# Optimization experiments

Hardware: AMD Instinct MI355X
Metric: run time of the kernel (lower is better)

Reference implementation:

```python
import jax, jax.numpy as jnp
import numpy as np

T, B, C = 256, 512, 128
NA = 4  # num attentions


def _lin(key, fan_in, fan_out):
    kw, kb = jax.random.split(key)
    s = 1.0 / np.sqrt(fan_in)
    W = jax.random.uniform(kw, (fan_in, fan_out), jnp.float32, -s, s)
    b = jax.random.uniform(kb, (fan_out,), jnp.float32, -s, s)
    return W, b


def setup_inputs() -> dict:
    key = jax.random.key(0)
    ks = jax.random.split(key, 12)
    inp = {
        'eeg': jax.random.normal(ks[0], (T, B, C), jnp.float32),
        'eog': jax.random.normal(ks[1], (T, B, C), jnp.float32),
    }
    # LSTHM (shared across both modalities)
    inp['Ww'], inp['Wb'] = _lin(ks[2], C, 4 * C)
    inp['Uw'], inp['Ub'] = _lin(ks[3], C, 4 * C)
    inp['Vw'], inp['Vb'] = _lin(ks[4], C, 4 * C)
    # attention model: Linear(256,128) -> tanh -> Linear(128,1024)
    inp['A1'], inp['a1'] = _lin(ks[5], 2 * C, C)
    inp['A2'], inp['a2'] = _lin(ks[6], C, NA * 2 * C)
    # dim-reduce nets: Linear(512,128) -> tanh -> Linear(128,128), one per modality
    inp['D10'], inp['e10'] = _lin(ks[7], NA * C, C)
    inp['D20'], inp['e20'] = _lin(ks[8], C, C)
    inp['D11'], inp['e11'] = _lin(ks[9], NA * C, C)
    inp['D21'], inp['e21'] = _lin(ks[10], C, C)
    return inp


def reference(eeg, eog, Ww, Wb, Uw, Ub, Vw, Vb, A1, a1, A2, a2,
              D10, e10, D20, e20, D11, e11, D21, e21):
    def mlp(x, W1, b1, W2, b2):
        return jnp.tanh(x @ W1 + b1) @ W2 + b2

    def lsthm(x, c, h, z, first):
        # at t=0 the torch code zeroes the U/V affines entirely (biases included)
        sums = (x @ Ww + Wb) + jnp.where(first, 0.0, (h @ Uw + Ub) + (z @ Vw + Vb))
        f = jax.nn.sigmoid(sums[:, :C])
        i = jax.nn.sigmoid(sums[:, C:2 * C])
        o = jax.nn.sigmoid(sums[:, 2 * C:3 * C])
        ch = jnp.tanh(sums[:, 3 * C:])
        c_t = f * c + i * ch
        h_t = jnp.tanh(c_t) * o
        return c_t, h_t

    def step(carry, inp):
        c0, h0, c1, h1, z0, z1 = carry
        x0, x1, first = inp
        c0, h0 = lsthm(x0, c0, h0, z0, first)
        c1, h1 = lsthm(x1, c1, h1, z1, first)
        in_t = jnp.concatenate([h0, h1], axis=1)                       # [B, 2C]
        logits = mlp(in_t, A1, a1, A2, a2)                             # [B, NA*2C]
        atts = jax.nn.softmax(logits.reshape(-1, NA, 2 * C), axis=1)   # softmax over attentions
        atts = atts.reshape(-1, NA * 2 * C)
        out_t = jnp.concatenate([jnp.tile(h0, (1, NA)), jnp.tile(h1, (1, NA))], axis=1)
        att = atts * out_t                                             # [B, NA*2C]
        z0 = mlp(att[:, :NA * C], D10, e10, D20, e20)
        z1 = mlp(att[:, NA * C:], D11, e11, D21, e21)
        out = jnp.concatenate([z0, z1], axis=1)                        # [B, 2C]
        return (c0, h0, c1, h1, z0, z1), out

    zeros = jnp.zeros((eeg.shape[1], C), eeg.dtype)
    first = jnp.arange(eeg.shape[0]) == 0
    _, outs = jax.lax.scan(step, (zeros,) * 6, (eeg, eog, first))
    return outs  # [T, B, 2C]
```

## Files before the change

kernel.cpp:

```cpp
#include <hip/hip_runtime.h>

typedef unsigned short u16;
typedef unsigned int   u32;
typedef __attribute__((ext_vector_type(8))) __bf16 bf16x8;
typedef __attribute__((ext_vector_type(4))) float  f32x4;

#define T_STEPS 256
#define BATCH   512
#define RB      16
#define NBLK    32

__device__ __forceinline__ float b2f(u16 u){
  union { u32 i; float f; } v; v.i = ((u32)u) << 16; return v.f;
}
__device__ __forceinline__ u16 f2b(float f){
  u32 x = __float_as_uint(f);
  return (u16)((x + 0x7fffu + ((x >> 16) & 1u)) >> 16);
}
__device__ __forceinline__ float sigm_f(float x){ return 1.f/(1.f + __expf(-x)); }
__device__ __forceinline__ float tanh_f(float x){
  x = fminf(15.f, fmaxf(-15.f, x));
  float e = __expf(2.f*x);
  return (e - 1.f)/(e + 1.f);
}
__device__ __forceinline__ f32x4 MF(bf16x8 a, bf16x8 b, f32x4 c){
  return __builtin_amdgcn_mfma_f32_16x16x32_bf16(a, b, c, 0, 0, 0);
}

__device__ __forceinline__ bf16x8 frA(const u16* buf, int l, int kc, int RS){
  int r = l & 15;
  int byte = r*RS + kc*64 + ((l >> 4) << 4);
  byte ^= (r & 7) << 4;
  return *(const bf16x8*)((const char*)buf + byte);
}
__device__ __forceinline__ void st16(u16* buf, int r, int c, u16 v, int RS){
  int byte = r*RS + c*2; byte ^= (r & 7) << 4;
  *(u16*)((char*)buf + byte) = v;
}
__device__ __forceinline__ float ld16f(const u16* buf, int r, int c, int RS){
  int byte = r*RS + c*2; byte ^= (r & 7) << 4;
  return b2f(*(const u16*)((const char*)buf + byte));
}
__device__ __forceinline__ void st16x4(u16* buf, int r, int c, ushort4 v, int RS){
  int byte = r*RS + c*2; byte ^= (r & 7) << 4;
  *(ushort4*)((char*)buf + byte) = v;
}
__device__ __forceinline__ bf16x8 frB(const u16* pk, int nt, int kt, int KT, int l){
  return *(const bf16x8*)(pk + ((((nt*KT + kt) << 6) + l) << 3));
}

__global__ void pack_w(const float* __restrict__ src, u16* __restrict__ dst,
                       int Ksrc, int N, int ktOff, int KT)
{
  int i = blockIdx.x*256 + threadIdx.x;
  if (i >= Ksrc*N) return;
  int j = i & 7, l = (i >> 3) & 63, p = i >> 9;
  int nkt = Ksrc >> 5;
  int kt = p % nkt, nt = p / nkt;
  int k = (kt << 5) + ((l >> 4) << 3) + j;
  int n = (nt << 4) + (l & 15);
  dst[(((nt*KT + ktOff + kt) << 6) + l)*8 + j] = f2b(src[(size_t)k*N + n]);
}

__global__ void pack_bias(const float* Wb, const float* Ub, const float* Vb,
                          const float* a1, const float* a2,
                          const float* e10, const float* e20,
                          const float* e11, const float* e21, float* bout)
{
  int i = blockIdx.x*256 + threadIdx.x;
  if (i >= 2688) return;
  float v;
  if      (i < 512)  v = Wb[i];
  else if (i < 1024) { int n = i - 512; v = Wb[n] + Ub[n] + Vb[n]; }
  else if (i < 1152) v = a1[i - 1024];
  else if (i < 2176) v = a2[i - 1152];
  else if (i < 2304) v = e10[i - 2176];
  else if (i < 2432) v = e20[i - 2304];
  else if (i < 2560) v = e11[i - 2432];
  else               v = e21[i - 2560];
  bout[i] = v;
}

__global__ __launch_bounds__(512, 2) void marn_mfma5(
  const float* __restrict__ eeg, const float* __restrict__ eog,
  const u16* __restrict__ UVWt, const u16* __restrict__ A1t,
  const u16* __restrict__ A2t,  const u16* __restrict__ D10t,
  const u16* __restrict__ D20t, const u16* __restrict__ D11t,
  const u16* __restrict__ D21t, const float* __restrict__ bias,
  float* __restrict__ out)
{
  __shared__ u16  aS1[2][16*384];
  __shared__ u16  aS2a[16*256];
  __shared__ u16  aS2b[16*128];
  __shared__ u16  aS3a[2][16*512];
  __shared__ u16  aS3b[2][16*128];
  __shared__ float bsh[2688];

  const int tid = threadIdx.x;
  const int w = tid >> 6, l = tid & 63;
  const int hi = l >> 4, li = l & 15;
  const int r0 = blockIdx.x * RB;

  for (int i = tid; i < 2688; i += 512) bsh[i] = bias[i];
  for (int i = tid; i < 2*16*384; i += 512) ((u16*)aS1)[i] = 0;
  float cst[2][4] = {{0,0,0,0},{0,0,0,0}};

  const int xi = tid << 3;
  const int xm = xi >> 11, xrr = (xi >> 7) & 15, xc = xi & 127;
  const float* xsrc = (xm ? eog : eeg) + ((size_t)(r0 + xrr))*128 + xc;
  f32x4 xa = __builtin_nontemporal_load((const f32x4*)xsrc);
  f32x4 xb = __builtin_nontemporal_load((const f32x4*)(xsrc + 4));
  __syncthreads();
  {
    ushort4 va, vb;
    va.x = f2b(xa[0]); va.y = f2b(xa[1]); va.z = f2b(xa[2]); va.w = f2b(xa[3]);
    vb.x = f2b(xb[0]); vb.y = f2b(xb[1]); vb.z = f2b(xb[2]); vb.w = f2b(xb[3]);
    st16x4(&aS1[xm][0], xrr, xc,     va, 768);
    st16x4(&aS1[xm][0], xrr, xc + 4, vb, 768);
  }
  __syncthreads();

  for (int t = 0; t < T_STEPS; ++t){
    f32x4 ac0[4] = {{0,0,0,0},{0,0,0,0},{0,0,0,0},{0,0,0,0}};
    f32x4 ac1[4] = {{0,0,0,0},{0,0,0,0},{0,0,0,0},{0,0,0,0}};
    {
      #pragma unroll
      for (int kc = 0; kc < 12; ++kc){
        bf16x8 fa0 = frA(&aS1[0][0], l, kc, 768);
        bf16x8 fa1 = frA(&aS1[1][0], l, kc, 768);
        #pragma unroll
        for (int g = 0; g < 4; ++g){
          bf16x8 b = frB(UVWt, w + 8*g, kc, 12, l);
          ac0[g] = MF(fa0, b, ac0[g]);
          ac1[g] = MF(fa1, b, ac1[g]);
        }
      }
    }
    __syncthreads();

    {
      const float* bg = bsh + (t == 0 ? 0 : 512);
      const int col = w*16 + li;
      #pragma unroll
      for (int jr = 0; jr < 4; ++jr){
        const int row = hi*4 + jr;
        {
          float f  = sigm_f(ac0[0][jr] + bg[col]);
          float ii = sigm_f(ac0[1][jr] + bg[128+col]);
          float o  = sigm_f(ac0[2][jr] + bg[256+col]);
          float ch = tanh_f(ac0[3][jr] + bg[384+col]);
          cst[0][jr] = f*cst[0][jr] + ii*ch;
          u16 hb = f2b(tanh_f(cst[0][jr])*o);
          st16(&aS1[0][0], row, 128 + col, hb, 768);
          st16(aS2a, row, col, hb, 512);
        }
        {
          float f  = sigm_f(ac1[0][jr] + bg[col]);
          float ii = sigm_f(ac1[1][jr] + bg[128+col]);
          float o  = sigm_f(ac1[2][jr] + bg[256+col]);
          float ch = tanh_f(ac1[3][jr] + bg[384+col]);
          cst[1][jr] = f*cst[1][jr] + ii*ch;
          u16 hb = f2b(tanh_f(cst[1][jr])*o);
          st16(&aS1[1][0], row, 128 + col, hb, 768);
          st16(aS2a, row, 128 + col, hb, 512);
        }
      }
    }
    __syncthreads();

    {
      f32x4 acc = {0,0,0,0};
      #pragma unroll
      for (int kc = 0; kc < 8; ++kc)
        acc = MF(frA(aS2a, l, kc, 512), frB(A1t, w, kc, 8, l), acc);
      const int col = w*16 + li;
      #pragma unroll
      for (int jr = 0; jr < 4; ++jr)
        st16(aS2b, hi*4 + jr, col, f2b(tanh_f(acc[jr] + bsh[1024 + col])), 256);
    }
    __syncthreads();

    {
      int tn = (t + 1 < T_STEPS) ? t + 1 : t;
      xa = __builtin_nontemporal_load((const f32x4*)(xsrc + (size_t)tn*BATCH*128));
      xb = __builtin_nontemporal_load((const f32x4*)(xsrc + (size_t)tn*BATCH*128 + 4));
    }

    {
      bf16x8 yf[4];
      #pragma unroll
      for (int kc = 0; kc < 4; ++kc) yf[kc] = frA(aS2b, l, kc, 256);
      const float* a2f = bsh + 1152;
      #pragma unroll
      for (int gq = 0; gq < 2; ++gq){
        const int gb = w + 8*gq;
        f32x4 q0 = {0,0,0,0}, q1 = {0,0,0,0}, q2 = {0,0,0,0}, q3 = {0,0,0,0};
        #pragma unroll
        for (int kc = 0; kc < 4; ++kc){
          q0 = MF(yf[kc], frB(A2t, gb,      kc, 4, l), q0);
          q1 = MF(yf[kc], frB(A2t, gb + 16, kc, 4, l), q1);
          q2 = MF(yf[kc], frB(A2t, gb + 32, kc, 4, l), q2);
          q3 = MF(yf[kc], frB(A2t, gb + 48, kc, 4, l), q3);
        }
        const int g = gb*16 + li;
        #pragma unroll
        for (int jr = 0; jr < 4; ++jr){
          const int row = hi*4 + jr;
          float v0 = q0[jr] + a2f[g];
          float v1 = q1[jr] + a2f[256 + g];
          float v2 = q2[jr] + a2f[512 + g];
          float v3 = q3[jr] + a2f[768 + g];
          float mx = fmaxf(fmaxf(v0,v1), fmaxf(v2,v3));
          float e0 = __expf(v0-mx), e1 = __expf(v1-mx);
          float e2 = __expf(v2-mx), e3 = __expf(v3-mx);
          float inv = 1.f/(e0+e1+e2+e3);
          float h0v = ld16f(aS2a, row, g & 127, 512);
          float h1v = ld16f(aS2a, row, 128 + (g & 127), 512);
          st16(&aS3a[0][0], row, g,       f2b(e0*inv*h0v), 1024);
          st16(&aS3a[0][0], row, 256 + g, f2b(e1*inv*h0v), 1024);
          st16(&aS3a[1][0], row, g,       f2b(e2*inv*h1v), 1024);
          st16(&aS3a[1][0], row, 256 + g, f2b(e3*inv*h1v), 1024);
        }
      }
    }
    __syncthreads();

    {
      #pragma unroll
      for (int m = 0; m < 2; ++m){
        const u16* Dt = m ? D11t : D10t;
        f32x4 acc = {0,0,0,0};
        #pragma unroll
        for (int kc = 0; kc < 16; ++kc)
          acc = MF(frA(&aS3a[m][0], l, kc, 1024), frB(Dt, w, kc, 16, l), acc);
        const int col = w*16 + li;
        const float* e1f = bsh + (m ? 2432 : 2176);
        #pragma unroll
        for (int jr = 0; jr < 4; ++jr)
          st16(&aS3b[m][0], hi*4 + jr, col, f2b(tanh_f(acc[jr] + e1f[col])), 256);
      }
    }
    __syncthreads();

    {
      #pragma unroll
      for (int m = 0; m < 2; ++m){
        const u16* Dt = m ? D21t : D20t;
        f32x4 acc = {0,0,0,0};
        #pragma unroll
        for (int kc = 0; kc < 4; ++kc)
          acc = MF(frA(&aS3b[m][0], l, kc, 256), frB(Dt, w, kc, 4, l), acc);
        const int col = w*16 + li;
        const float* e2f = bsh + (m ? 2560 : 2304);
        #pragma unroll
        for (int jr = 0; jr < 4; ++jr){
          const int row = hi*4 + jr;
          float z = acc[jr] + e2f[col];
          __builtin_nontemporal_store(z, &out[((size_t)t*BATCH + r0 + row)*256 + m*128 + col]);
          st16(&aS1[m][0], row, 256 + col, f2b(z), 768);
        }
      }
    }
    {
      ushort4 va, vb;
      va.x = f2b(xa[0]); va.y = f2b(xa[1]); va.z = f2b(xa[2]); va.w = f2b(xa[3]);
      vb.x = f2b(xb[0]); vb.y = f2b(xb[1]); vb.z = f2b(xb[2]); vb.w = f2b(xb[3]);
      st16x4(&aS1[xm][0], xrr, xc,     va, 768);
      st16x4(&aS1[xm][0], xrr, xc + 4, vb, 768);
    }
    __syncthreads();
  }
}

extern "C" void kernel_launch(void* const* d_in, const int* in_sizes, int n_in,
                              void* d_out, int out_size, void* d_ws, size_t ws_size,
                              hipStream_t stream)
{
  const float* eeg = (const float*)d_in[0];
  const float* eog = (const float*)d_in[1];
  const float* Ww  = (const float*)d_in[2];
  const float* Wb  = (const float*)d_in[3];
  const float* Uw  = (const float*)d_in[4];
  const float* Ub  = (const float*)d_in[5];
  const float* Vw  = (const float*)d_in[6];
  const float* Vb  = (const float*)d_in[7];
  const float* A1  = (const float*)d_in[8];
  const float* a1  = (const float*)d_in[9];
  const float* A2  = (const float*)d_in[10];
  const float* a2  = (const float*)d_in[11];
  const float* D10 = (const float*)d_in[12];
  const float* e10 = (const float*)d_in[13];
  const float* D20 = (const float*)d_in[14];
  const float* e20 = (const float*)d_in[15];
  const float* D11 = (const float*)d_in[16];
  const float* e11 = (const float*)d_in[17];
  const float* D21 = (const float*)d_in[18];
  const float* e21 = (const float*)d_in[19];

  char* ws = (char*)d_ws;
  u16*  UVWt = (u16*)(ws);
  u16*  A1t  = (u16*)(ws + 393216);
  u16*  A2t  = (u16*)(ws + 458752);
  u16*  D10t = (u16*)(ws + 720896);
  u16*  D20t = (u16*)(ws + 851968);
  u16*  D11t = (u16*)(ws + 884736);
  u16*  D21t = (u16*)(ws + 1015808);
  float* bias = (float*)(ws + 1048576);

  auto nb = [](int n){ return dim3((unsigned)((n + 255)/256)); };
  pack_w<<<nb(65536),  256, 0, stream>>>(Ww,  UVWt, 128, 512,  0, 12);
  pack_w<<<nb(65536),  256, 0, stream>>>(Uw,  UVWt, 128, 512,  4, 12);
  pack_w<<<nb(65536),  256, 0, stream>>>(Vw,  UVWt, 128, 512,  8, 12);
  pack_w<<<nb(32768),  256, 0, stream>>>(A1,  A1t,  256, 128,  0, 8);
  pack_w<<<nb(131072), 256, 0, stream>>>(A2,  A2t,  128, 1024, 0, 4);
  pack_w<<<nb(65536),  256, 0, stream>>>(D10, D10t, 512, 128,  0, 16);
  pack_w<<<nb(16384),  256, 0, stream>>>(D20, D20t, 128, 128,  0, 4);
  pack_w<<<nb(65536),  256, 0, stream>>>(D11, D11t, 512, 128,  0, 16);
  pack_w<<<nb(16384),  256, 0, stream>>>(D21, D21t, 128, 128,  0, 4);
  pack_bias<<<nb(2688), 256, 0, stream>>>(Wb, Ub, Vb, a1, a2, e10, e20, e11, e21, bias);

  marn_mfma5<<<NBLK, 512, 0, stream>>>(eeg, eog, UVWt, A1t, A2t,
                                       D10t, D20t, D11t, D21t, bias, (float*)d_out);
}
```

Baseline: 7.106 ms.

## Prefetch weight fragments into registers across barriers and use LDS-only barrier waits

Global weight fragments for each GEMM stage (UVW, A1, A2, D1x, D2x) are now loaded into registers one phase ahead, before the preceding barrier, so their latency overlaps the previous stage's compute. The UVW loop is double-buffered in blocks of three k-chunks. __syncthreads is replaced by a barrier that waits only on LDS counters, so outstanding global loads need not drain. The cost is much higher register pressure, which under launch_bounds(512,2) could cause spills.

New measurement: 7.105 ms. About the same (-0.0%).

```diff
diff --git a/kernel.cpp b/kernel.cpp
--- a/kernel.cpp
+++ b/kernel.cpp
@@ -25,6 +25,10 @@
 }
 __device__ __forceinline__ f32x4 MF(bf16x8 a, bf16x8 b, f32x4 c){
   return __builtin_amdgcn_mfma_f32_16x16x32_bf16(a, b, c, 0, 0, 0);
+}
+__device__ __forceinline__ void BAR(){
+  asm volatile("s_waitcnt lgkmcnt(0)" ::: "memory");
+  __builtin_amdgcn_s_barrier();
 }
 
 __device__ __forceinline__ bf16x8 frA(const u16* buf, int l, int kc, int RS){
@@ -81,7 +85,7 @@
   bout[i] = v;
 }
 
-__global__ __launch_bounds__(512, 2) void marn_mfma5(
+__global__ __launch_bounds__(512, 2) void marn_mfma6(
   const float* __restrict__ eeg, const float* __restrict__ eog,
   const u16* __restrict__ UVWt, const u16* __restrict__ A1t,
   const u16* __restrict__ A2t,  const u16* __restrict__ D10t,
@@ -124,19 +128,40 @@
     f32x4 ac0[4] = {{0,0,0,0},{0,0,0,0},{0,0,0,0},{0,0,0,0}};
     f32x4 ac1[4] = {{0,0,0,0},{0,0,0,0},{0,0,0,0},{0,0,0,0}};
     {
-      #pragma unroll
-      for (int kc = 0; kc < 12; ++kc){
-        bf16x8 fa0 = frA(&aS1[0][0], l, kc, 768);
-        bf16x8 fa1 = frA(&aS1[1][0], l, kc, 768);
-        #pragma unroll
-        for (int g = 0; g < 4; ++g){
-          bf16x8 b = frB(UVWt, w + 8*g, kc, 12, l);
-          ac0[g] = MF(fa0, b, ac0[g]);
-          ac1[g] = MF(fa1, b, ac1[g]);
-        }
-      }
-    }
-    __syncthreads();
+      bf16x8 wb0[12], wb1[12];
+      #pragma unroll
+      for (int j = 0; j < 3; ++j)
+        #pragma unroll
+        for (int g = 0; g < 4; ++g)
+          wb0[j*4+g] = frB(UVWt, w + 8*g, j, 12, l);
+      #pragma unroll
+      for (int blk = 0; blk < 4; ++blk){
+        bf16x8* cur = (blk & 1) ? wb1 : wb0;
+        bf16x8* nxt = (blk & 1) ? wb0 : wb1;
+        if (blk < 3){
+          #pragma unroll
+          for (int j = 0; j < 3; ++j)
+            #pragma unroll
+            for (int g = 0; g < 4; ++g)
+              nxt[j*4+g] = frB(UVWt, w + 8*g, 3*blk + 3 + j, 12, l);
+        }
+        #pragma unroll
+        for (int j = 0; j < 3; ++j){
+          const int kc = 3*blk + j;
+          bf16x8 fa0 = frA(&aS1[0][0], l, kc, 768);
+          bf16x8 fa1 = frA(&aS1[1][0], l, kc, 768);
+          #pragma unroll
+          for (int g = 0; g < 4; ++g){
+            ac0[g] = MF(fa0, cur[j*4+g], ac0[g]);
+            ac1[g] = MF(fa1, cur[j*4+g], ac1[g]);
+          }
+        }
+      }
+    }
+    bf16x8 wa1[8];
+    #pragma unroll
+    for (int kc = 0; kc < 8; ++kc) wa1[kc] = frB(A1t, w, kc, 8, l);
+    BAR();
 
     {
       const float* bg = bsh + (t == 0 ? 0 : 512);
@@ -166,50 +191,63 @@
         }
       }
     }
-    __syncthreads();
+    bf16x8 wa2A[16];
+    #pragma unroll
+    for (int s = 0; s < 4; ++s)
+      #pragma unroll
+      for (int kc = 0; kc < 4; ++kc)
+        wa2A[s*4+kc] = frB(A2t, w + 16*s, kc, 4, l);
+    BAR();
 
     {
       f32x4 acc = {0,0,0,0};
       #pragma unroll
       for (int kc = 0; kc < 8; ++kc)
-        acc = MF(frA(aS2a, l, kc, 512), frB(A1t, w, kc, 8, l), acc);
+        acc = MF(frA(aS2a, l, kc, 512), wa1[kc], acc);
       const int col = w*16 + li;
       #pragma unroll
       for (int jr = 0; jr < 4; ++jr)
         st16(aS2b, hi*4 + jr, col, f2b(tanh_f(acc[jr] + bsh[1024 + col])), 256);
     }
-    __syncthreads();
-
+    bf16x8 wa2B[16];
+    #pragma unroll
+    for (int s = 0; s < 4; ++s)
+      #pragma unroll
+      for (int kc = 0; kc < 4; ++kc)
+        wa2B[s*4+kc] = frB(A2t, w + 8 + 16*s, kc, 4, l);
     {
       int tn = (t + 1 < T_STEPS) ? t + 1 : t;
       xa = __builtin_nontemporal_load((const f32x4*)(xsrc + (size_t)tn*BATCH*128));
       xb = __builtin_nontemporal_load((const f32x4*)(xsrc + (size_t)tn*BATCH*128 + 4));
     }
+    BAR();
 
     {
       bf16x8 yf[4];
       #pragma unroll
       for (int kc = 0; kc < 4; ++kc) yf[kc] = frA(aS2b, l, kc, 256);
       const float* a2f = bsh + 1152;
+      f32x4 qq[8];
+      #pragma unroll
+      for (int s = 0; s < 8; ++s) qq[s] = (f32x4){0,0,0,0};
+      #pragma unroll
+      for (int s = 0; s < 4; ++s)
+        #pragma unroll
+        for (int kc = 0; kc < 4; ++kc){
+          qq[s]     = MF(yf[kc], wa2A[s*4+kc], qq[s]);
+          qq[4 + s] = MF(yf[kc], wa2B[s*4+kc], qq[4 + s]);
+        }
       #pragma unroll
       for (int gq = 0; gq < 2; ++gq){
         const int gb = w + 8*gq;
-        f32x4 q0 = {0,0,0,0}, q1 = {0,0,0,0}, q2 = {0,0,0,0}, q3 = {0,0,0,0};
-        #pragma unroll
-        for (int kc = 0; kc < 4; ++kc){
-          q0 = MF(yf[kc], frB(A2t, gb,      kc, 4, l), q0);
-          q1 = MF(yf[kc], frB(A2t, gb + 16, kc, 4, l), q1);
-          q2 = MF(yf[kc], frB(A2t, gb + 32, kc, 4, l), q2);
-          q3 = MF(yf[kc], frB(A2t, gb + 48, kc, 4, l), q3);
-        }
         const int g = gb*16 + li;
         #pragma unroll
         for (int jr = 0; jr < 4; ++jr){
           const int row = hi*4 + jr;
-          float v0 = q0[jr] + a2f[g];
-          float v1 = q1[jr] + a2f[256 + g];
-          float v2 = q2[jr] + a2f[512 + g];
-          float v3 = q3[jr] + a2f[768 + g];
+          float v0 = qq[4*gq + 0][jr] + a2f[g];
+          float v1 = qq[4*gq + 1][jr] + a2f[256 + g];
+          float v2 = qq[4*gq + 2][jr] + a2f[512 + g];
+          float v3 = qq[4*gq + 3][jr] + a2f[768 + g];
           float mx = fmaxf(fmaxf(v0,v1), fmaxf(v2,v3));
           float e0 = __expf(v0-mx), e1 = __expf(v1-mx);
           float e2 = __expf(v2-mx), e3 = __expf(v3-mx);
@@ -223,41 +261,73 @@
         }
       }
     }
-    __syncthreads();
-
-    {
-      #pragma unroll
-      for (int m = 0; m < 2; ++m){
-        const u16* Dt = m ? D11t : D10t;
+    bf16x8 wd0[16];
+    #pragma unroll
+    for (int kc = 0; kc < 16; ++kc) wd0[kc] = frB(D10t, w, kc, 16, l);
+    BAR();
+
+    {
+      bf16x8 wd1[16];
+      #pragma unroll
+      for (int kc = 0; kc < 16; ++kc) wd1[kc] = frB(D11t, w, kc, 16, l);
+      const int col = w*16 + li;
+      {
         f32x4 acc = {0,0,0,0};
         #pragma unroll
         for (int kc = 0; kc < 16; ++kc)
-          acc = MF(frA(&aS3a[m][0], l, kc, 1024), frB(Dt, w, kc, 16, l), acc);
-        const int col = w*16 + li;
-        const float* e1f = bsh + (m ? 2432 : 2176);
+          acc = MF(frA(&aS3a[0][0], l, kc, 1024), wd0[kc], acc);
+        const float* e1f = bsh + 2176;
         #pragma unroll
         for (int jr = 0; jr < 4; ++jr)
-          st16(&aS3b[m][0], hi*4 + jr, col, f2b(tanh_f(acc[jr] + e1f[col])), 256);
-      }
-    }
-    __syncthreads();
-
-    {
-      #pragma unroll
-      for (int m = 0; m < 2; ++m){
-        const u16* Dt = m ? D21t : D20t;
+          st16(&aS3b[0][0], hi*4 + jr, col, f2b(tanh_f(acc[jr] + e1f[col])), 256);
+      }
+      {
         f32x4 acc = {0,0,0,0};
         #pragma unroll
+        for (int kc = 0; kc < 16; ++kc)
+          acc = MF(frA(&aS3a[1][0], l, kc, 1024), wd1[kc], acc);
+        const float* e1f = bsh + 2432;
+        #pragma unroll
+        for (int jr = 0; jr < 4; ++jr)
+          st16(&aS3b[1][0], hi*4 + jr, col, f2b(tanh_f(acc[jr] + e1f[col])), 256);
+      }
+    }
+    bf16x8 wd2m0[4], wd2m1[4];
+    #pragma unroll
+    for (int kc = 0; kc < 4; ++kc){
+      wd2m0[kc] = frB(D20t, w, kc, 4, l);
+      wd2m1[kc] = frB(D21t, w, kc, 4, l);
+    }
+    BAR();
+
+    {
+      const int col = w*16 + li;
+      {
+        f32x4 acc = {0,0,0,0};
+        #pragma unroll
         for (int kc = 0; kc < 4; ++kc)
-          acc = MF(frA(&aS3b[m][0], l, kc, 256), frB(Dt, w, kc, 4, l), acc);
-        const int col = w*16 + li;
-        const float* e2f = bsh + (m ? 2560 : 2304);
+          acc = MF(frA(&aS3b[0][0], l, kc, 256), wd2m0[kc], acc);
+        const float* e2f = bsh + 2304;
         #pragma unroll
         for (int jr = 0; jr < 4; ++jr){
           const int row = hi*4 + jr;
           float z = acc[jr] + e2f[col];
-          __builtin_nontemporal_store(z, &out[((size_t)t*BATCH + r0 + row)*256 + m*128 + col]);
-          st16(&aS1[m][0], row, 256 + col, f2b(z), 768);
+          __builtin_nontemporal_store(z, &out[((size_t)t*BATCH + r0 + row)*256 + col]);
+          st16(&aS1[0][0], row, 256 + col, f2b(z), 768);
+        }
+      }
+      {
+        f32x4 acc = {0,0,0,0};
+        #pragma unroll
+        for (int kc = 0; kc < 4; ++kc)
+          acc = MF(frA(&aS3b[1][0], l, kc, 256), wd2m1[kc], acc);
+        const float* e2f = bsh + 2560;
+        #pragma unroll
+        for (int jr = 0; jr < 4; ++jr){
+          const int row = hi*4 + jr;
+          float z = acc[jr] + e2f[col];
+          __builtin_nontemporal_store(z, &out[((size_t)t*BATCH + r0 + row)*256 + 128 + col]);
+          st16(&aS1[1][0], row, 256 + col, f2b(z), 768);
         }
       }
     }
@@ -268,7 +338,7 @@
       st16x4(&aS1[xm][0], xrr, xc,     va, 768);
       st16x4(&aS1[xm][0], xrr, xc + 4, vb, 768);
     }
-    __syncthreads();
+    BAR();
   }
 }
 
@@ -319,6 +389,6 @@
   pack_w<<<nb(16384),  256, 0, stream>>>(D21, D21t, 128, 128,  0, 4);
   pack_bias<<<nb(2688), 256, 0, stream>>>(Wb, Ub, Vb, a1, a2, e10, e20, e11, e21, bias);
 
-  marn_mfma5<<<NBLK, 512, 0, stream>>>(eeg, eog, UVWt, A1t, A2t,
+  marn_mfma6<<<NBLK, 512, 0, stream>>>(eeg, eog, UVWt, A1t, A2t,
                                        D10t, D20t, D11t, D21t, bias, (float*)d_out);
 }
```

## Stream weights through per-wave LDS ring via async global-to-LDS DMA

Applied to the files above, without the earlier changes.

Replaces direct global loads of packed weight fragments with a per-wave double-buffered LDS ring filled by global_load_lds DMA. Each k-chunk's weights are prefetched two chunks ahead across every stage, including across timesteps. The code manages this with explicit vmcnt/lgkmcnt waits and raw s_barrier in place of __syncthreads. Biases now live in registers instead of a shared array, and the next-timestep input prefetch is moved into the D1 stage. This aims to hide the L2 latency of the weight reads on the serial recurrence, at the cost of fragile hand-counted waitcnt logic and an extra 64KB of LDS.

After: 6.608 ms. -7.0%, faster.

```diff
diff --git a/kernel.cpp b/kernel.cpp
--- a/kernel.cpp
+++ b/kernel.cpp
@@ -9,6 +9,9 @@
 #define BATCH   512
 #define RB      16
 #define NBLK    32
+
+#define WAITV(N) asm volatile("s_waitcnt vmcnt(" #N ")" ::: "memory")
+#define LGKM0    asm volatile("s_waitcnt lgkmcnt(0)" ::: "memory")
 
 __device__ __forceinline__ float b2f(u16 u){
   union { u32 i; float f; } v; v.i = ((u32)u) << 16; return v.f;
@@ -26,6 +29,31 @@
 __device__ __forceinline__ f32x4 MF(bf16x8 a, bf16x8 b, f32x4 c){
   return __builtin_amdgcn_mfma_f32_16x16x32_bf16(a, b, c, 0, 0, 0);
 }
+__device__ __forceinline__ void BAR(){
+  asm volatile("s_waitcnt lgkmcnt(0)" ::: "memory");
+  __builtin_amdgcn_s_barrier();
+}
+
+__device__ __forceinline__ void dma16(const u16* g, u16* l){
+  __builtin_amdgcn_global_load_lds(
+      (const __attribute__((address_space(1))) void*)g,
+      (__attribute__((address_space(3))) void*)l, 16, 0, 0);
+}
+__device__ __forceinline__ void issueG(const u16* f0, const u16* f1,
+                                       const u16* f2, const u16* f3,
+                                       u16* ringW, int par, int l){
+  u16* s = ringW + par*2048;
+  dma16(f0 + l*8, s);
+  dma16(f1 + l*8, s + 512);
+  dma16(f2 + l*8, s + 1024);
+  dma16(f3 + l*8, s + 1536);
+}
+__device__ __forceinline__ const u16* fp(const u16* pk, int nt, int kt, int KT){
+  return pk + (size_t)(nt*KT + kt)*512;
+}
+__device__ __forceinline__ bf16x8 rdW(const u16* ringW, int par, int j, int l){
+  return *(const bf16x8*)(ringW + par*2048 + j*512 + l*8);
+}
 
 __device__ __forceinline__ bf16x8 frA(const u16* buf, int l, int kc, int RS){
   int r = l & 15;
@@ -44,9 +72,6 @@
 __device__ __forceinline__ void st16x4(u16* buf, int r, int c, ushort4 v, int RS){
   int byte = r*RS + c*2; byte ^= (r & 7) << 4;
   *(ushort4*)((char*)buf + byte) = v;
-}
-__device__ __forceinline__ bf16x8 frB(const u16* pk, int nt, int kt, int KT, int l){
-  return *(const bf16x8*)(pk + ((((nt*KT + kt) << 6) + l) << 3));
 }
 
 __global__ void pack_w(const float* __restrict__ src, u16* __restrict__ dst,
@@ -81,7 +106,7 @@
   bout[i] = v;
 }
 
-__global__ __launch_bounds__(512, 2) void marn_mfma5(
+__global__ __launch_bounds__(512, 2) void marn_dma(
   const float* __restrict__ eeg, const float* __restrict__ eog,
   const u16* __restrict__ UVWt, const u16* __restrict__ A1t,
   const u16* __restrict__ A2t,  const u16* __restrict__ D10t,
@@ -89,21 +114,35 @@
   const u16* __restrict__ D21t, const float* __restrict__ bias,
   float* __restrict__ out)
 {
-  __shared__ u16  aS1[2][16*384];
-  __shared__ u16  aS2a[16*256];
-  __shared__ u16  aS2b[16*128];
-  __shared__ u16  aS3a[2][16*512];
-  __shared__ u16  aS3b[2][16*128];
-  __shared__ float bsh[2688];
+  __shared__ u16 aS1[2][16*384];
+  __shared__ u16 aS2a[16*256];
+  __shared__ u16 aS2b[16*128];
+  __shared__ u16 aS3a[2][16*512];
+  __shared__ u16 aS3b[2][16*128];
+  __shared__ u16 ring[8][4096];
 
   const int tid = threadIdx.x;
   const int w = tid >> 6, l = tid & 63;
   const int hi = l >> 4, li = l & 15;
   const int r0 = blockIdx.x * RB;
-
-  for (int i = tid; i < 2688; i += 512) bsh[i] = bias[i];
+  u16* ringW = &ring[w][0];
+
   for (int i = tid; i < 2*16*384; i += 512) ((u16*)aS1)[i] = 0;
   float cst[2][4] = {{0,0,0,0},{0,0,0,0}};
+
+  const int col = w*16 + li;
+  const int g1c = (w + 8)*16 + li;
+  float bW[4], bA[4], a2b0[4], a2b1[4];
+  #pragma unroll
+  for (int q = 0; q < 4; ++q){
+    bW[q]   = bias[q*128 + col];
+    bA[q]   = bias[512 + q*128 + col];
+    a2b0[q] = bias[1152 + q*256 + col];
+    a2b1[q] = bias[1152 + q*256 + g1c];
+  }
+  const float a1b  = bias[1024 + col];
+  const float e1b0 = bias[2176 + col], e1b1 = bias[2432 + col];
+  const float e2b0 = bias[2304 + col], e2b1 = bias[2560 + col];
 
   const int xi = tid << 3;
   const int xm = xi >> 11, xrr = (xi >> 7) & 15, xc = xi & 127;
@@ -120,45 +159,56 @@
   }
   __syncthreads();
 
+  issueG(fp(UVWt,w,0,12), fp(UVWt,w+8,0,12), fp(UVWt,w+16,0,12), fp(UVWt,w+24,0,12), ringW, 0, l);
+  issueG(fp(UVWt,w,1,12), fp(UVWt,w+8,1,12), fp(UVWt,w+16,1,12), fp(UVWt,w+24,1,12), ringW, 1, l);
+
   for (int t = 0; t < T_STEPS; ++t){
     f32x4 ac0[4] = {{0,0,0,0},{0,0,0,0},{0,0,0,0},{0,0,0,0}};
     f32x4 ac1[4] = {{0,0,0,0},{0,0,0,0},{0,0,0,0},{0,0,0,0}};
-    {
-      #pragma unroll
-      for (int kc = 0; kc < 12; ++kc){
-        bf16x8 fa0 = frA(&aS1[0][0], l, kc, 768);
-        bf16x8 fa1 = frA(&aS1[1][0], l, kc, 768);
-        #pragma unroll
-        for (int g = 0; g < 4; ++g){
-          bf16x8 b = frB(UVWt, w + 8*g, kc, 12, l);
-          ac0[g] = MF(fa0, b, ac0[g]);
-          ac1[g] = MF(fa1, b, ac1[g]);
-        }
-      }
-    }
-    __syncthreads();
-
-    {
-      const float* bg = bsh + (t == 0 ? 0 : 512);
-      const int col = w*16 + li;
+    #pragma unroll
+    for (int kc = 0; kc < 12; ++kc){
+      WAITV(4);
+      bf16x8 b0 = rdW(ringW, kc&1, 0, l);
+      bf16x8 b1 = rdW(ringW, kc&1, 1, l);
+      bf16x8 b2 = rdW(ringW, kc&1, 2, l);
+      bf16x8 b3 = rdW(ringW, kc&1, 3, l);
+      bf16x8 fa0 = frA(&aS1[0][0], l, kc, 768);
+      bf16x8 fa1 = frA(&aS1[1][0], l, kc, 768);
+      ac0[0] = MF(fa0, b0, ac0[0]);  ac1[0] = MF(fa1, b0, ac1[0]);
+      ac0[1] = MF(fa0, b1, ac0[1]);  ac1[1] = MF(fa1, b1, ac1[1]);
+      ac0[2] = MF(fa0, b2, ac0[2]);  ac1[2] = MF(fa1, b2, ac1[2]);
+      ac0[3] = MF(fa0, b3, ac0[3]);  ac1[3] = MF(fa1, b3, ac1[3]);
+      LGKM0;
+      if (kc < 10){
+        const int k2 = kc + 2;
+        issueG(fp(UVWt,w,k2,12), fp(UVWt,w+8,k2,12), fp(UVWt,w+16,k2,12), fp(UVWt,w+24,k2,12), ringW, k2&1, l);
+      } else if (kc == 10){
+        issueG(fp(A1t,w,0,8), fp(A1t,w,1,8), fp(A1t,w,2,8), fp(A1t,w,3,8), ringW, 0, l);
+      } else {
+        issueG(fp(A1t,w,4,8), fp(A1t,w,5,8), fp(A1t,w,6,8), fp(A1t,w,7,8), ringW, 1, l);
+      }
+    }
+    BAR();
+
+    {
       #pragma unroll
       for (int jr = 0; jr < 4; ++jr){
         const int row = hi*4 + jr;
         {
-          float f  = sigm_f(ac0[0][jr] + bg[col]);
-          float ii = sigm_f(ac0[1][jr] + bg[128+col]);
-          float o  = sigm_f(ac0[2][jr] + bg[256+col]);
-          float ch = tanh_f(ac0[3][jr] + bg[384+col]);
+          float f  = sigm_f(ac0[0][jr] + (t==0 ? bW[0] : bA[0]));
+          float ii = sigm_f(ac0[1][jr] + (t==0 ? bW[1] : bA[1]));
+          float o  = sigm_f(ac0[2][jr] + (t==0 ? bW[2] : bA[2]));
+          float ch = tanh_f(ac0[3][jr] + (t==0 ? bW[3] : bA[3]));
           cst[0][jr] = f*cst[0][jr] + ii*ch;
           u16 hb = f2b(tanh_f(cst[0][jr])*o);
           st16(&aS1[0][0], row, 128 + col, hb, 768);
           st16(aS2a, row, col, hb, 512);
         }
         {
-          float f  = sigm_f(ac1[0][jr] + bg[col]);
-          float ii = sigm_f(ac1[1][jr] + bg[128+col]);
-          float o  = sigm_f(ac1[2][jr] + bg[256+col]);
-          float ch = tanh_f(ac1[3][jr] + bg[384+col]);
+          float f  = sigm_f(ac1[0][jr] + (t==0 ? bW[0] : bA[0]));
+          float ii = sigm_f(ac1[1][jr] + (t==0 ? bW[1] : bA[1]));
+          float o  = sigm_f(ac1[2][jr] + (t==0 ? bW[2] : bA[2]));
+          float ch = tanh_f(ac1[3][jr] + (t==0 ? bW[3] : bA[3]));
           cst[1][jr] = f*cst[1][jr] + ii*ch;
           u16 hb = f2b(tanh_f(cst[1][jr])*o);
           st16(&aS1[1][0], row, 128 + col, hb, 768);
@@ -166,50 +216,63 @@
         }
       }
     }
-    __syncthreads();
-
-    {
-      f32x4 acc = {0,0,0,0};
-      #pragma unroll
-      for (int kc = 0; kc < 8; ++kc)
-        acc = MF(frA(aS2a, l, kc, 512), frB(A1t, w, kc, 8, l), acc);
-      const int col = w*16 + li;
+    BAR();
+
+    {
+      f32x4 accA = {0,0,0,0};
+      WAITV(4);
+      #pragma unroll
+      for (int j = 0; j < 4; ++j)
+        accA = MF(frA(aS2a, l, j, 512), rdW(ringW, 0, j, l), accA);
+      LGKM0;
+      issueG(fp(A2t,w,0,4), fp(A2t,w,1,4), fp(A2t,w,2,4), fp(A2t,w,3,4), ringW, 0, l);
+      WAITV(4);
+      #pragma unroll
+      for (int j = 0; j < 4; ++j)
+        accA = MF(frA(aS2a, l, 4+j, 512), rdW(ringW, 1, j, l), accA);
+      LGKM0;
+      issueG(fp(A2t,w+16,0,4), fp(A2t,w+16,1,4), fp(A2t,w+16,2,4), fp(A2t,w+16,3,4), ringW, 1, l);
       #pragma unroll
       for (int jr = 0; jr < 4; ++jr)
-        st16(aS2b, hi*4 + jr, col, f2b(tanh_f(acc[jr] + bsh[1024 + col])), 256);
-    }
-    __syncthreads();
-
-    {
-      int tn = (t + 1 < T_STEPS) ? t + 1 : t;
-      xa = __builtin_nontemporal_load((const f32x4*)(xsrc + (size_t)tn*BATCH*128));
-      xb = __builtin_nontemporal_load((const f32x4*)(xsrc + (size_t)tn*BATCH*128 + 4));
-    }
+        st16(aS2b, hi*4 + jr, col, f2b(tanh_f(accA[jr] + a1b)), 256);
+    }
+    BAR();
 
     {
       bf16x8 yf[4];
       #pragma unroll
       for (int kc = 0; kc < 4; ++kc) yf[kc] = frA(aS2b, l, kc, 256);
-      const float* a2f = bsh + 1152;
+      f32x4 qq[8];
+      #pragma unroll
+      for (int s = 0; s < 8; ++s) qq[s] = (f32x4){0,0,0,0};
+      #pragma unroll
+      for (int j = 0; j < 8; ++j){
+        WAITV(4);
+        #pragma unroll
+        for (int kc = 0; kc < 4; ++kc)
+          qq[j] = MF(yf[kc], rdW(ringW, j&1, kc, l), qq[j]);
+        LGKM0;
+        if (j < 6){
+          const int j2 = j + 2;
+          const int nt = (j2 < 4) ? (w + 16*j2) : (w + 8 + 16*(j2 - 4));
+          issueG(fp(A2t,nt,0,4), fp(A2t,nt,1,4), fp(A2t,nt,2,4), fp(A2t,nt,3,4), ringW, j2&1, l);
+        } else if (j == 6){
+          issueG(fp(D10t,w,0,16), fp(D10t,w,1,16), fp(D10t,w,2,16), fp(D10t,w,3,16), ringW, 0, l);
+        } else {
+          issueG(fp(D10t,w,4,16), fp(D10t,w,5,16), fp(D10t,w,6,16), fp(D10t,w,7,16), ringW, 1, l);
+        }
+      }
       #pragma unroll
       for (int gq = 0; gq < 2; ++gq){
-        const int gb = w + 8*gq;
-        f32x4 q0 = {0,0,0,0}, q1 = {0,0,0,0}, q2 = {0,0,0,0}, q3 = {0,0,0,0};
-        #pragma unroll
-        for (int kc = 0; kc < 4; ++kc){
-          q0 = MF(yf[kc], frB(A2t, gb,      kc, 4, l), q0);
-          q1 = MF(yf[kc], frB(A2t, gb + 16, kc, 4, l), q1);
-          q2 = MF(yf[kc], frB(A2t, gb + 32, kc, 4, l), q2);
-          q3 = MF(yf[kc], frB(A2t, gb + 48, kc, 4, l), q3);
-        }
-        const int g = gb*16 + li;
+        const int g = (w + 8*gq)*16 + li;
+        const float* ab = gq ? a2b1 : a2b0;
         #pragma unroll
         for (int jr = 0; jr < 4; ++jr){
           const int row = hi*4 + jr;
-          float v0 = q0[jr] + a2f[g];
-          float v1 = q1[jr] + a2f[256 + g];
-          float v2 = q2[jr] + a2f[512 + g];
-          float v3 = q3[jr] + a2f[768 + g];
+          float v0 = qq[4*gq + 0][jr] + ab[0];
+          float v1 = qq[4*gq + 1][jr] + ab[1];
+          float v2 = qq[4*gq + 2][jr] + ab[2];
+          float v3 = qq[4*gq + 3][jr] + ab[3];
           float mx = fmaxf(fmaxf(v0,v1), fmaxf(v2,v3));
           float e0 = __expf(v0-mx), e1 = __expf(v1-mx);
           float e2 = __expf(v2-mx), e3 = __expf(v3-mx);
@@ -223,43 +286,74 @@
         }
       }
     }
-    __syncthreads();
-
-    {
-      #pragma unroll
-      for (int m = 0; m < 2; ++m){
-        const u16* Dt = m ? D11t : D10t;
-        f32x4 acc = {0,0,0,0};
+    BAR();
+
+    {
+      f32x4 au0 = {0,0,0,0}, au1 = {0,0,0,0};
+      #pragma unroll
+      for (int j = 0; j < 8; ++j){
+        if (j < 2) { WAITV(4); } else { WAITV(6); }
+        const u16* src = (j < 4) ? &aS3a[0][0] : &aS3a[1][0];
         #pragma unroll
-        for (int kc = 0; kc < 16; ++kc)
-          acc = MF(frA(&aS3a[m][0], l, kc, 1024), frB(Dt, w, kc, 16, l), acc);
-        const int col = w*16 + li;
-        const float* e1f = bsh + (m ? 2432 : 2176);
-        #pragma unroll
-        for (int jr = 0; jr < 4; ++jr)
-          st16(&aS3b[m][0], hi*4 + jr, col, f2b(tanh_f(acc[jr] + e1f[col])), 256);
-      }
-    }
-    __syncthreads();
-
-    {
-      #pragma unroll
-      for (int m = 0; m < 2; ++m){
-        const u16* Dt = m ? D21t : D20t;
-        f32x4 acc = {0,0,0,0};
-        #pragma unroll
-        for (int kc = 0; kc < 4; ++kc)
-          acc = MF(frA(&aS3b[m][0], l, kc, 256), frB(Dt, w, kc, 4, l), acc);
-        const int col = w*16 + li;
-        const float* e2f = bsh + (m ? 2560 : 2304);
-        #pragma unroll
-        for (int jr = 0; jr < 4; ++jr){
-          const int row = hi*4 + jr;
-          float z = acc[jr] + e2f[col];
-          __builtin_nontemporal_store(z, &out[((size_t)t*BATCH + r0 + row)*256 + m*128 + col]);
-          st16(&aS1[m][0], row, 256 + col, f2b(z), 768);
-        }
-      }
+        for (int i = 0; i < 4; ++i){
+          bf16x8 a = frA(src, l, (j&3)*4 + i, 1024);
+          bf16x8 b = rdW(ringW, j&1, i, l);
+          if (j < 4) au0 = MF(a, b, au0); else au1 = MF(a, b, au1);
+        }
+        LGKM0;
+        if (j < 6){
+          const int j2 = j + 2;
+          const u16* Dt = (j2 < 4) ? D10t : D11t;
+          const int ktb = (j2 & 3)*4;
+          issueG(fp(Dt,w,ktb,16), fp(Dt,w,ktb+1,16), fp(Dt,w,ktb+2,16), fp(Dt,w,ktb+3,16), ringW, j2&1, l);
+        } else if (j == 6){
+          issueG(fp(D20t,w,0,4), fp(D20t,w,1,4), fp(D20t,w,2,4), fp(D20t,w,3,4), ringW, 0, l);
+        } else {
+          issueG(fp(D21t,w,0,4), fp(D21t,w,1,4), fp(D21t,w,2,4), fp(D21t,w,3,4), ringW, 1, l);
+        }
+        if (j == 1){
+          int tn = (t + 1 < T_STEPS) ? t + 1 : t;
+          xa = __builtin_nontemporal_load((const f32x4*)(xsrc + (size_t)tn*BATCH*128));
+          xb = __builtin_nontemporal_load((const f32x4*)(xsrc + (size_t)tn*BATCH*128 + 4));
+        }
+      }
+      #pragma unroll
+      for (int jr = 0; jr < 4; ++jr){
+        st16(&aS3b[0][0], hi*4 + jr, col, f2b(tanh_f(au0[jr] + e1b0)), 256);
+        st16(&aS3b[1][0], hi*4 + jr, col, f2b(tanh_f(au1[jr] + e1b1)), 256);
+      }
+    }
+    BAR();
+
+    {
+      WAITV(4);
+      f32x4 az0 = {0,0,0,0};
+      #pragma unroll
+      for (int kc = 0; kc < 4; ++kc)
+        az0 = MF(frA(&aS3b[0][0], l, kc, 256), rdW(ringW, 0, kc, l), az0);
+      #pragma unroll
+      for (int jr = 0; jr < 4; ++jr){
+        const int row = hi*4 + jr;
+        float z = az0[jr] + e2b0;
+        __builtin_nontemporal_store(z, &out[((size_t)t*BATCH + r0 + row)*256 + col]);
+        st16(&aS1[0][0], row, 256 + col, f2b(z), 768);
+      }
+      LGKM0;
+      issueG(fp(UVWt,w,0,12), fp(UVWt,w+8,0,12), fp(UVWt,w+16,0,12), fp(UVWt,w+24,0,12), ringW, 0, l);
+      WAITV(8);
+      f32x4 az1 = {0,0,0,0};
+      #pragma unroll
+      for (int kc = 0; kc < 4; ++kc)
+        az1 = MF(frA(&aS3b[1][0], l, kc, 256), rdW(ringW, 1, kc, l), az1);
+      #pragma unroll
+      for (int jr = 0; jr < 4; ++jr){
+        const int row = hi*4 + jr;
+        float z = az1[jr] + e2b1;
+        __builtin_nontemporal_store(z, &out[((size_t)t*BATCH + r0 + row)*256 + 128 + col]);
+        st16(&aS1[1][0], row, 256 + col, f2b(z), 768);
+      }
+      LGKM0;
+      issueG(fp(UVWt,w,1,12), fp(UVWt,w+8,1,12), fp(UVWt,w+16,1,12), fp(UVWt,w+24,1,12), ringW, 1, l);
     }
     {
       ushort4 va, vb;
@@ -268,7 +362,7 @@
       st16x4(&aS1[xm][0], xrr, xc,     va, 768);
       st16x4(&aS1[xm][0], xrr, xc + 4, vb, 768);
     }
-    __syncthreads();
+    BAR();
   }
 }
 
@@ -319,6 +413,6 @@
   pack_w<<<nb(16384),  256, 0, stream>>>(D21, D21t, 128, 128,  0, 4);
   pack_bias<<<nb(2688), 256, 0, stream>>>(Wb, Ub, Vb, a1, a2, e10, e20, e11, e21, bias);
 
-  marn_mfma5<<<NBLK, 512, 0, stream>>>(eeg, eog, UVWt, A1t, A2t,
-                                       D10t, D20t, D11t, D21t, bias, (float*)d_out);
-}
+  marn_dma<<<NBLK, 512, 0, stream>>>(eeg, eog, UVWt, A1t, A2t,
+                                     D10t, D20t, D11t, D21t, bias, (float*)d_out);
+}
```
